# Kernel optimization log

Hardware: AMD Instinct MI355X
Metric: run time of the kernel (lower is better)

The kernel has to match this reference:

```python
import jax, jax.numpy as jnp
import numpy as np

N_NODES = 100000
N_EDGES = 1600000
D_FEAT = 48
K = 10
ALPHA = 0.1


def setup_inputs() -> dict:
    key = jax.random.key(0)
    k1, k2, k3 = jax.random.split(key, 3)
    x = jax.random.normal(k1, (N_NODES, D_FEAT), dtype=jnp.float32)
    edge_index = jax.random.randint(k2, (2, N_EDGES), 0, N_NODES, dtype=jnp.int64)
    edge_weight = jax.random.uniform(k3, (N_EDGES,), dtype=jnp.float32)
    return {"x": x, "edge_index": edge_index, "edge_weight": edge_weight}


def reference(x, edge_index, edge_weight):
    row, col = edge_index[0], edge_index[1]
    # degree-weighted normalization: w_ij / sum_j w_ij
    deg_w = jax.ops.segment_sum(edge_weight, row, num_segments=N_NODES)
    norm = edge_weight / (deg_w[row] + 1e-10)  # [E]

    def step(h, _):
        # gather h at source-of-message (col), scale, scatter-add to row
        msg = jax.ops.segment_sum(norm[:, None] * h[col], row, num_segments=N_NODES)
        h_new = (1.0 - ALPHA) * msg + ALPHA * x
        return h_new, None

    h, _ = jax.lax.scan(step, x, None, length=K)
    return h
```

## Files before the change

kernel.cpp:

```cpp
#include <hip/hip_runtime.h>
#include <hip/hip_fp16.h>

#define N_NODES 100000
#define N_EDGES 1600000
#define K_ITER 10

#define TPN 6
#define NPB 32
#define PAD 4

#define NBUCK 391
#define BROWS 256
#define BSTRIDE 4608
#define BK_TB 512
#define BK_EPT 16
#define BK_SEG (BK_TB * BK_EPT)
#define BK_NB ((N_EDGES + BK_SEG - 1) / BK_SEG)

typedef unsigned int u32;
typedef unsigned long long u64;

__global__ __launch_bounds__(BK_TB) void k_bucket(const int* __restrict__ row,
        const int* __restrict__ col, const float* __restrict__ w,
        u32* __restrict__ bcursor, u64* __restrict__ bedge, int E) {
    __shared__ u32 hcnt[NBUCK], sbase[NBUCK];
    int t = threadIdx.x;
    for (int b = t; b < NBUCK; b += BK_TB) hcnt[b] = 0;
    __syncthreads();
    int i0 = blockIdx.x * BK_SEG + t;
#pragma unroll
    for (int k = 0; k < BK_EPT; ++k) {
        int i = i0 + k * BK_TB;
        if (i < E) atomicAdd(&hcnt[((u32)row[i]) >> 8], 1u);
    }
    __syncthreads();
    for (int b = t; b < NBUCK; b += BK_TB) {
        u32 c = hcnt[b];
        sbase[b] = c ? atomicAdd(&bcursor[b], c) : 0u;
        hcnt[b] = 0;
    }
    __syncthreads();
#pragma unroll
    for (int k = 0; k < BK_EPT; ++k) {
        int i = i0 + k * BK_TB;
        if (i < E) {
            u32 r = (u32)row[i];
            u32 b = r >> 8;
            u32 rk = atomicAdd(&hcnt[b], 1u);
            u32 idx = sbase[b] + rk;
            if (idx < BSTRIDE)
                bedge[(u64)b * BSTRIDE + idx] =
                    ((u64)(r & 255u) << 32) | ((u64)(u32)col[i] << 15) |
                    (u64)(__float_as_uint(w[i]) >> 17);
        }
    }
}

__global__ __launch_bounds__(BROWS) void k_buildA(const u32* __restrict__ bcursor,
        const u64* __restrict__ bedge, u32* __restrict__ cntarr,
        u32* __restrict__ bsum) {
    __shared__ u32 cnt[BROWS];
    __shared__ u32 sh[BROWS];
    int b = blockIdx.x, t = threadIdx.x;
    cnt[t] = 0;
    __syncthreads();
    u32 cb = bcursor[b];
    if (cb > BSTRIDE) cb = BSTRIDE;
    const u64* be = bedge + (u64)b * BSTRIDE;
    for (u32 j = t; j < cb; j += BROWS)
        atomicAdd(&cnt[(u32)(be[j] >> 32) & 255u], 1u);
    __syncthreads();
    u32 c = cnt[t];
    cntarr[b * BROWS + t] = c;
    sh[t] = (c + PAD - 1) & ~(u32)(PAD - 1);
    __syncthreads();
    for (int off = 128; off > 0; off >>= 1) {
        if (t < off) sh[t] += sh[t + off];
        __syncthreads();
    }
    if (t == 0) bsum[b] = sh[0];
}

__global__ void k_scanbk(const u32* __restrict__ bsum, u32* __restrict__ bbase,
                         int* __restrict__ rowptr) {
    __shared__ u32 sh[512];
    int t = threadIdx.x;
    u32 v = (t < NBUCK) ? bsum[t] : 0;
    sh[t] = v;
    __syncthreads();
    for (int off = 1; off < 512; off <<= 1) {
        u32 u = (t >= off) ? sh[t - off] : 0;
        __syncthreads();
        sh[t] += u;
        __syncthreads();
    }
    if (t < NBUCK) bbase[t] = sh[t] - v;
    if (t == NBUCK - 1) rowptr[N_NODES] = (int)sh[t];
}

__global__ __launch_bounds__(BROWS) void k_buildB(const u32* __restrict__ bcursor,
        const u64* __restrict__ bedge, const u32* __restrict__ cntarr,
        const u32* __restrict__ bbase, int* __restrict__ rowptr,
        u32* __restrict__ epack, float* __restrict__ scale) {
    __shared__ u32 sh[BROWS];
    __shared__ u32 run[BROWS];
    __shared__ float swsum[BROWS];
    int b = blockIdx.x, t = threadIdx.x;
    u32 c = cntarr[b * BROWS + t];
    u32 p = (c + PAD - 1) & ~(u32)(PAD - 1);
    sh[t] = p;
    __syncthreads();
    for (int off = 1; off < BROWS; off <<= 1) {
        u32 u = (t >= off) ? sh[t - off] : 0;
        __syncthreads();
        sh[t] += u;
        __syncthreads();
    }
    u32 my = bbase[b] + sh[t] - p;
    int grow = b * BROWS + t;
    if (grow < N_NODES) rowptr[grow] = (int)my;
    run[t] = my;
    swsum[t] = 0.f;
    __syncthreads();
    u32 cb = bcursor[b];
    if (cb > BSTRIDE) cb = BSTRIDE;
    const u64* be = bedge + (u64)b * BSTRIDE;
    for (u32 j = t; j < cb; j += BROWS) {
        u64 e = be[j];
        u32 r = (u32)(e >> 32) & 255u;
        u32 pk = (u32)e;
        u32 pos = atomicAdd(&run[r], 1u);
        epack[pos] = pk;
        atomicAdd(&swsum[r], __uint_as_float((pk & 0x7fffu) << 17));
    }
    __syncthreads();
    if (grow < N_NODES) scale[grow] = 0.9f / (swsum[t] + 1e-10f);
}

__global__ void k_x2h(const float4* __restrict__ x, float4* __restrict__ x16) {
    int i = blockIdx.x * blockDim.x + threadIdx.x;
    int n = i / TPN, c = i % TPN;
    if (n >= N_NODES) return;
    float4 a = x[n * 12 + 2 * c], b = x[n * 12 + 2 * c + 1];
    float4 o;
    ((__half2*)&o)[0] = __floats2half2_rn(a.x, a.y);
    ((__half2*)&o)[1] = __floats2half2_rn(a.z, a.w);
    ((__half2*)&o)[2] = __floats2half2_rn(b.x, b.y);
    ((__half2*)&o)[3] = __floats2half2_rn(b.z, b.w);
    x16[(n << 3) + c] = o;
}

#define PFMA(UU, HV, AA, BB)                                                  \
    {                                                                         \
        float wv = __uint_as_float(((UU) & 0x7fffu) << 17) * sc;              \
        float2 f0 = __half22float2(*(__half2*)&HV.x);                         \
        float2 f1 = __half22float2(*(__half2*)&HV.y);                         \
        float2 f2 = __half22float2(*(__half2*)&HV.z);                         \
        float2 f3 = __half22float2(*(__half2*)&HV.w);                         \
        AA.x += wv * f0.x; AA.y += wv * f0.y; AA.z += wv * f1.x; AA.w += wv * f1.y; \
        BB.x += wv * f2.x; BB.y += wv * f2.y; BB.z += wv * f3.x; BB.w += wv * f3.y; \
    }

template <int LAST>
__global__ __launch_bounds__(192) void k_pull(const int* __restrict__ rowptr,
                                              const u32* __restrict__ epack,
                                              const float* __restrict__ scale,
                                              const float4* __restrict__ x,
                                              const float4* __restrict__ src16,
                                              void* __restrict__ dstv) {
    int node = blockIdx.x * NPB + threadIdx.x / TPN;
    int c = threadIdx.x % TPN;
    if (node >= N_NODES) return;
    int beg = rowptr[node], end = rowptr[node + 1];
    float sc = scale[node];
    float4 xa = x[node * 12 + 2 * c], xb = x[node * 12 + 2 * c + 1];
    float4 A0 = make_float4(0.1f * xa.x, 0.1f * xa.y, 0.1f * xa.z, 0.1f * xa.w);
    float4 B0 = make_float4(0.1f * xb.x, 0.1f * xb.y, 0.1f * xb.z, 0.1f * xb.w);
    float4 A1 = make_float4(0, 0, 0, 0), B1 = make_float4(0, 0, 0, 0);
    if (beg < end) {
        uint4 p = *(const uint4*)(epack + beg);
        float4 h0 = src16[((p.x >> 15) << 3) + c];
        float4 h1 = src16[((p.y >> 15) << 3) + c];
        float4 h2 = src16[((p.z >> 15) << 3) + c];
        float4 h3 = src16[((p.w >> 15) << 3) + c];
        for (int e = beg + 4; e < end; e += 4) {
            uint4 pn = *(const uint4*)(epack + e);
            float4 g0 = src16[((pn.x >> 15) << 3) + c];
            float4 g1 = src16[((pn.y >> 15) << 3) + c];
            float4 g2 = src16[((pn.z >> 15) << 3) + c];
            float4 g3 = src16[((pn.w >> 15) << 3) + c];
            PFMA(p.x, h0, A0, B0) PFMA(p.y, h1, A1, B1)
            PFMA(p.z, h2, A0, B0) PFMA(p.w, h3, A1, B1)
            p = pn; h0 = g0; h1 = g1; h2 = g2; h3 = g3;
        }
        PFMA(p.x, h0, A0, B0) PFMA(p.y, h1, A1, B1)
        PFMA(p.z, h2, A0, B0) PFMA(p.w, h3, A1, B1)
    }
    float4 RA = make_float4(A0.x + A1.x, A0.y + A1.y, A0.z + A1.z, A0.w + A1.w);
    float4 RB = make_float4(B0.x + B1.x, B0.y + B1.y, B0.z + B1.z, B0.w + B1.w);
    if (LAST) {
        float4* out = (float4*)dstv;
        out[node * 12 + 2 * c]     = RA;
        out[node * 12 + 2 * c + 1] = RB;
    } else {
        float4 o;
        ((__half2*)&o)[0] = __floats2half2_rn(RA.x, RA.y);
        ((__half2*)&o)[1] = __floats2half2_rn(RA.z, RA.w);
        ((__half2*)&o)[2] = __floats2half2_rn(RB.x, RB.y);
        ((__half2*)&o)[3] = __floats2half2_rn(RB.z, RB.w);
        ((float4*)dstv)[(node << 3) + c] = o;
    }
}

extern "C" void kernel_launch(void* const* d_in, const int* in_sizes, int n_in,
                              void* d_out, int out_size, void* d_ws, size_t ws_size,
                              hipStream_t stream) {
    const float* x  = (const float*)d_in[0];
    const int*   ei = (const int*)d_in[1];
    const float* w  = (const float*)d_in[2];
    const int E = in_sizes[2];
    const int* row = ei;
    const int* col = ei + E;

    char* ws = (char*)d_ws;
    int*    rowptr  = (int*)(ws);
    float*  scale   = (float*)(ws + 400032);
    u32*    bsum    = (u32*)(ws + 800032);
    u32*    bbase   = (u32*)(ws + 801600);
    u32*    bcursor = (u32*)(ws + 803168);
    u32*    cntarr  = (u32*)(ws + 804736);
    u32*    epack   = (u32*)(ws + 1205120);
    u64*    bedge   = (u64*)(ws + 8805184);
    float4* hB16    = (float4*)(ws + 14852352);
    float4* hA16    = (float4*)d_out;

    const int pgrid = N_NODES / NPB;
    const int xgrid = (N_NODES * TPN + 191) / 192;

    hipMemsetAsync(bcursor, 0, NBUCK * sizeof(u32), stream);
    hipMemsetAsync(epack, 0, (size_t)(N_EDGES + 3 * N_NODES + 16) * sizeof(u32), stream);
    k_bucket<<<BK_NB, BK_TB, 0, stream>>>(row, col, w, bcursor, bedge, E);
    k_buildA<<<NBUCK, BROWS, 0, stream>>>(bcursor, bedge, cntarr, bsum);
    k_scanbk<<<1, 512, 0, stream>>>(bsum, bbase, rowptr);
    k_buildB<<<NBUCK, BROWS, 0, stream>>>(bcursor, bedge, cntarr, bbase,
                                          rowptr, epack, scale);
    k_x2h  <<<xgrid, 192, 0, stream>>>((const float4*)x, hA16);

    float4* src = hA16;
    float4* dst = hB16;
    for (int k = 1; k <= K_ITER - 1; ++k) {
        k_pull<0><<<pgrid, NPB * TPN, 0, stream>>>(rowptr, epack, scale,
                                                   (const float4*)x, src, dst);
        float4* t = src; src = dst; dst = t;
    }
    k_pull<1><<<pgrid, NPB * TPN, 0, stream>>>(rowptr, epack, scale,
                                               (const float4*)x, src, d_out);
}
```

Measured before the change: 442.8 us.

## Order each row's edges by coarse column partition to improve gather locality

```diff
diff --git a/kernel.cpp b/kernel.cpp
--- a/kernel.cpp
+++ b/kernel.cpp
@@ -16,6 +16,8 @@
 #define BK_EPT 16
 #define BK_SEG (BK_TB * BK_EPT)
 #define BK_NB ((N_EDGES + BK_SEG - 1) / BK_SEG)
+
+#define NPART 16
 
 typedef unsigned int u32;
 typedef unsigned long long u64;
@@ -57,22 +59,34 @@
 }
 
 __global__ __launch_bounds__(BROWS) void k_buildA(const u32* __restrict__ bcursor,
-        const u64* __restrict__ bedge, u32* __restrict__ cntarr,
+        const u64* __restrict__ bedge, uint4* __restrict__ cnt16,
         u32* __restrict__ bsum) {
-    __shared__ u32 cnt[BROWS];
+    __shared__ u32 cnt[NPART * BROWS];
     __shared__ u32 sh[BROWS];
     int b = blockIdx.x, t = threadIdx.x;
-    cnt[t] = 0;
+#pragma unroll
+    for (int k = 0; k < NPART; ++k) cnt[k * BROWS + t] = 0;
     __syncthreads();
     u32 cb = bcursor[b];
     if (cb > BSTRIDE) cb = BSTRIDE;
     const u64* be = bedge + (u64)b * BSTRIDE;
-    for (u32 j = t; j < cb; j += BROWS)
-        atomicAdd(&cnt[(u32)(be[j] >> 32) & 255u], 1u);
-    __syncthreads();
-    u32 c = cnt[t];
-    cntarr[b * BROWS + t] = c;
-    sh[t] = (c + PAD - 1) & ~(u32)(PAD - 1);
+    for (u32 j = t; j < cb; j += BROWS) {
+        u64 e = be[j];
+        u32 r = (u32)(e >> 32) & 255u;
+        u32 p = ((u32)e) >> 28;
+        atomicAdd(&cnt[p * BROWS + r], 1u);
+    }
+    __syncthreads();
+    u32 c[NPART], tot = 0;
+#pragma unroll
+    for (int p = 0; p < NPART; ++p) { c[p] = cnt[p * BROWS + t]; tot += c[p]; }
+    uint4 pk;
+    pk.x = c[0] | (c[1] << 8) | (c[2] << 16) | (c[3] << 24);
+    pk.y = c[4] | (c[5] << 8) | (c[6] << 16) | (c[7] << 24);
+    pk.z = c[8] | (c[9] << 8) | (c[10] << 16) | (c[11] << 24);
+    pk.w = c[12] | (c[13] << 8) | (c[14] << 16) | (c[15] << 24);
+    cnt16[b * BROWS + t] = pk;
+    sh[t] = (tot + PAD - 1) & ~(u32)(PAD - 1);
     __syncthreads();
     for (int off = 128; off > 0; off >>= 1) {
         if (t < off) sh[t] += sh[t + off];
@@ -99,16 +113,24 @@
 }
 
 __global__ __launch_bounds__(BROWS) void k_buildB(const u32* __restrict__ bcursor,
-        const u64* __restrict__ bedge, const u32* __restrict__ cntarr,
+        const u64* __restrict__ bedge, const uint4* __restrict__ cnt16,
         const u32* __restrict__ bbase, int* __restrict__ rowptr,
         u32* __restrict__ epack, float* __restrict__ scale) {
     __shared__ u32 sh[BROWS];
-    __shared__ u32 run[BROWS];
+    __shared__ u32 run[BROWS * NPART];
     __shared__ float swsum[BROWS];
     int b = blockIdx.x, t = threadIdx.x;
-    u32 c = cntarr[b * BROWS + t];
-    u32 p = (c + PAD - 1) & ~(u32)(PAD - 1);
-    sh[t] = p;
+    uint4 pk = cnt16[b * BROWS + t];
+    u32 c[NPART];
+    c[0] = pk.x & 255u; c[1] = (pk.x >> 8) & 255u; c[2] = (pk.x >> 16) & 255u; c[3] = pk.x >> 24;
+    c[4] = pk.y & 255u; c[5] = (pk.y >> 8) & 255u; c[6] = (pk.y >> 16) & 255u; c[7] = pk.y >> 24;
+    c[8] = pk.z & 255u; c[9] = (pk.z >> 8) & 255u; c[10] = (pk.z >> 16) & 255u; c[11] = pk.z >> 24;
+    c[12] = pk.w & 255u; c[13] = (pk.w >> 8) & 255u; c[14] = (pk.w >> 16) & 255u; c[15] = pk.w >> 24;
+    u32 tot = 0;
+#pragma unroll
+    for (int p = 0; p < NPART; ++p) tot += c[p];
+    u32 ptot = (tot + PAD - 1) & ~(u32)(PAD - 1);
+    sh[t] = ptot;
     __syncthreads();
     for (int off = 1; off < BROWS; off <<= 1) {
         u32 u = (t >= off) ? sh[t - off] : 0;
@@ -116,10 +138,12 @@
         sh[t] += u;
         __syncthreads();
     }
-    u32 my = bbase[b] + sh[t] - p;
+    u32 my = bbase[b] + sh[t] - ptot;
     int grow = b * BROWS + t;
     if (grow < N_NODES) rowptr[grow] = (int)my;
-    run[t] = my;
+    u32 o = my;
+#pragma unroll
+    for (int p = 0; p < NPART; ++p) { run[t * NPART + p] = o; o += c[p]; }
     swsum[t] = 0.f;
     __syncthreads();
     u32 cb = bcursor[b];
@@ -128,10 +152,11 @@
     for (u32 j = t; j < cb; j += BROWS) {
         u64 e = be[j];
         u32 r = (u32)(e >> 32) & 255u;
-        u32 pk = (u32)e;
-        u32 pos = atomicAdd(&run[r], 1u);
-        epack[pos] = pk;
-        atomicAdd(&swsum[r], __uint_as_float((pk & 0x7fffu) << 17));
+        u32 pkv = (u32)e;
+        u32 p = pkv >> 28;
+        u32 pos = atomicAdd(&run[r * NPART + p], 1u);
+        epack[pos] = pkv;
+        atomicAdd(&swsum[r], __uint_as_float((pkv & 0x7fffu) << 17));
     }
     __syncthreads();
     if (grow < N_NODES) scale[grow] = 0.9f / (swsum[t] + 1e-10f);
@@ -228,9 +253,9 @@
     u32*    bsum    = (u32*)(ws + 800032);
     u32*    bbase   = (u32*)(ws + 801600);
     u32*    bcursor = (u32*)(ws + 803168);
-    u32*    cntarr  = (u32*)(ws + 804736);
-    u32*    epack   = (u32*)(ws + 1205120);
-    u64*    bedge   = (u64*)(ws + 8805184);
+    uint4*  cnt16   = (uint4*)(ws + 804736);
+    u32*    epack   = (u32*)(ws + 2406272);
+    u64*    bedge   = (u64*)(ws + 10006336);
     float4* hB16    = (float4*)(ws + 14852352);
     float4* hA16    = (float4*)d_out;
 
@@ -240,9 +265,9 @@
     hipMemsetAsync(bcursor, 0, NBUCK * sizeof(u32), stream);
     hipMemsetAsync(epack, 0, (size_t)(N_EDGES + 3 * N_NODES + 16) * sizeof(u32), stream);
     k_bucket<<<BK_NB, BK_TB, 0, stream>>>(row, col, w, bcursor, bedge, E);
-    k_buildA<<<NBUCK, BROWS, 0, stream>>>(bcursor, bedge, cntarr, bsum);
+    k_buildA<<<NBUCK, BROWS, 0, stream>>>(bcursor, bedge, cnt16, bsum);
     k_scanbk<<<1, 512, 0, stream>>>(bsum, bbase, rowptr);
-    k_buildB<<<NBUCK, BROWS, 0, stream>>>(bcursor, bedge, cntarr, bbase,
+    k_buildB<<<NBUCK, BROWS, 0, stream>>>(bcursor, bedge, cnt16, bbase,
                                           rowptr, epack, scale);
     k_x2h  <<<xgrid, 192, 0, stream>>>((const float4*)x, hA16);
 
```

New measurement: 429.8 us (median of 2 runs). 1.03x faster.
